# Optimization experiments

Measured on AMD Instinct MI355X. Metric: run time of the kernel, lower is better.

## Reference

```python
import jax, jax.numpy as jnp
import numpy as np

NUM_EXPERTS = 8
INTER = 2816   # moe_intermediate_size
DIM = 1024
T = 16         # flattened tokens
A = 2          # top-k experts per token


def setup_inputs() -> dict:
    key = jax.random.key(0)
    k_x, k_idx, k1, k2, k3 = jax.random.split(key, 5)
    x = jax.random.normal(k_x, (T, DIM), dtype=jnp.float32)
    expert_indices = jax.random.randint(k_idx, (T, A), 0, NUM_EXPERTS, dtype=jnp.int64)
    scale = 0.02
    w1 = jax.random.normal(k1, (NUM_EXPERTS, INTER, DIM), dtype=jnp.float32) * scale
    w2 = jax.random.normal(k2, (NUM_EXPERTS, DIM, INTER), dtype=jnp.float32) * scale
    w3 = jax.random.normal(k3, (NUM_EXPERTS, INTER, DIM), dtype=jnp.float32) * scale
    return {"x": x, "expert_indices": expert_indices, "w1": w1, "w2": w2, "w3": w3}


def reference(x, expert_indices, w1, w2, w3):
    # Gather per-token expert weights (same access pattern as the torch module).
    w1_g = w1[expert_indices]  # [T, A, INTER, DIM]
    w3_g = w3[expert_indices]  # [T, A, INTER, DIM]
    w2_g = w2[expert_indices]  # [T, A, DIM, INTER]
    # SwiGLU: silu(x @ w1^T) * (x @ w3^T), then project back with w2.
    x1 = jax.nn.silu(jnp.einsum('ti,taoi->tao', x, w1_g))  # [T, A, INTER]
    x3 = jnp.einsum('ti,taoi->tao', x, w3_g)               # [T, A, INTER]
    expert_outs = jnp.einsum('tao,taio->tai', x1 * x3, w2_g)  # [T, A, DIM]
    return expert_outs
```

## Files before the change

### kernel.cpp

```cpp
#include <hip/hip_runtime.h>
#include <math.h>

#define TOK   16
#define TOPA  2
#define NPAIR (TOK * TOPA)
#define DIM   1024
#define INTER 2816
#define NEXP  8

__device__ __forceinline__ unsigned pair_mask(const int* __restrict__ eidx, int e) {
    unsigned mask = 0;
    #pragma unroll
    for (int k = 0; k < NPAIR / 4; ++k) {
        const int4 v = ((const int4*)eidx)[k];
        mask |= (unsigned)(v.x == e) << (4 * k + 0);
        mask |= (unsigned)(v.y == e) << (4 * k + 1);
        mask |= (unsigned)(v.z == e) << (4 * k + 2);
        mask |= (unsigned)(v.w == e) << (4 * k + 3);
    }
    return mask;
}

__device__ __forceinline__ float dot4(float4 a, float4 b) {
    return a.x * b.x + a.y * b.y + a.z * b.z + a.w * b.w;
}

__global__ __launch_bounds__(256) void moe_gate_up(
    const float* __restrict__ x,
    const int*   __restrict__ eidx,
    const float* __restrict__ w1,
    const float* __restrict__ w3,
    float*       __restrict__ h)
{
    const int e = blockIdx.y;
    unsigned mask = pair_mask(eidx, e);
    if (!mask) return;

    const int tid  = threadIdx.x;
    const int lane = tid & 63;
    const int wave = tid >> 6;
    const int r0   = blockIdx.x * 8 + wave * 2;

    const float4* w1r = (const float4*)(w1 + ((size_t)e * INTER + r0) * DIM);
    const float4* w3r = (const float4*)(w3 + ((size_t)e * INTER + r0) * DIM);
    const float4* xb  = (const float4*)x;

    while (mask) {
        int p0 = __builtin_ctz(mask); mask &= mask - 1;
        int p1 = p0, p2 = p0, p3 = p0, nv = 1;
        if (mask) { p1 = __builtin_ctz(mask); mask &= mask - 1; nv = 2;
        if (mask) { p2 = __builtin_ctz(mask); mask &= mask - 1; nv = 3;
        if (mask) { p3 = __builtin_ctz(mask); mask &= mask - 1; nv = 4; } } }

        const float4* x0 = xb + (size_t)(p0 >> 1) * (DIM / 4);
        const float4* x1 = xb + (size_t)(p1 >> 1) * (DIM / 4);
        const float4* x2 = xb + (size_t)(p2 >> 1) * (DIM / 4);
        const float4* x3 = xb + (size_t)(p3 >> 1) * (DIM / 4);

        float s1[2][4], s3[2][4];
        #pragma unroll
        for (int r = 0; r < 2; ++r)
            #pragma unroll
            for (int j = 0; j < 4; ++j) { s1[r][j] = 0.f; s3[r][j] = 0.f; }

        #pragma unroll
        for (int k = 0; k < 4; ++k) {
            const float4 a0 = w1r[k * 64 + lane];
            const float4 a1 = w1r[256 + k * 64 + lane];
            const float4 b0 = w3r[k * 64 + lane];
            const float4 b1 = w3r[256 + k * 64 + lane];
            const float4 v0 = x0[k * 64 + lane];
            const float4 v1 = x1[k * 64 + lane];
            const float4 v2 = x2[k * 64 + lane];
            const float4 v3 = x3[k * 64 + lane];
            s1[0][0] += dot4(a0, v0); s1[0][1] += dot4(a0, v1);
            s1[0][2] += dot4(a0, v2); s1[0][3] += dot4(a0, v3);
            s1[1][0] += dot4(a1, v0); s1[1][1] += dot4(a1, v1);
            s1[1][2] += dot4(a1, v2); s1[1][3] += dot4(a1, v3);
            s3[0][0] += dot4(b0, v0); s3[0][1] += dot4(b0, v1);
            s3[0][2] += dot4(b0, v2); s3[0][3] += dot4(b0, v3);
            s3[1][0] += dot4(b1, v0); s3[1][1] += dot4(b1, v1);
            s3[1][2] += dot4(b1, v2); s3[1][3] += dot4(b1, v3);
        }

        #pragma unroll
        for (int off = 1; off < 64; off <<= 1) {
            #pragma unroll
            for (int r = 0; r < 2; ++r)
                #pragma unroll
                for (int j = 0; j < 4; ++j) {
                    s1[r][j] += __shfl_xor(s1[r][j], off);
                    s3[r][j] += __shfl_xor(s3[r][j], off);
                }
        }

        if (lane == 0) {
            const int pp[4] = { p0, p1, p2, p3 };
            #pragma unroll
            for (int j = 0; j < 4; ++j) {
                if (j < nv) {
                    #pragma unroll
                    for (int r = 0; r < 2; ++r) {
                        const float g = s1[r][j] / (1.f + __expf(-s1[r][j]));
                        h[(size_t)pp[j] * INTER + r0 + r] = g * s3[r][j];
                    }
                }
            }
        }
    }
}

__global__ __launch_bounds__(256) void moe_down(
    const float* __restrict__ h,
    const int*   __restrict__ eidx,
    const float* __restrict__ w2,
    float*       __restrict__ out)
{
    const int e = blockIdx.y;
    unsigned mask = pair_mask(eidx, e);
    if (!mask) return;

    const int tid  = threadIdx.x;
    const int lane = tid & 63;
    const int wave = tid >> 6;
    const int r0   = blockIdx.x * 8 + wave * 2;

    const float4* w2r = (const float4*)(w2 + ((size_t)e * DIM + r0) * INTER);
    const float4* hb  = (const float4*)h;

    while (mask) {
        int p0 = __builtin_ctz(mask); mask &= mask - 1;
        int p1 = p0, p2 = p0, p3 = p0, nv = 1;
        if (mask) { p1 = __builtin_ctz(mask); mask &= mask - 1; nv = 2;
        if (mask) { p2 = __builtin_ctz(mask); mask &= mask - 1; nv = 3;
        if (mask) { p3 = __builtin_ctz(mask); mask &= mask - 1; nv = 4; } } }

        const float4* h0 = hb + (size_t)p0 * (INTER / 4);
        const float4* h1 = hb + (size_t)p1 * (INTER / 4);
        const float4* h2 = hb + (size_t)p2 * (INTER / 4);
        const float4* h3 = hb + (size_t)p3 * (INTER / 4);

        float s[2][4];
        #pragma unroll
        for (int r = 0; r < 2; ++r)
            #pragma unroll
            for (int j = 0; j < 4; ++j) s[r][j] = 0.f;

        #pragma unroll
        for (int k = 0; k < 11; ++k) {
            const float4 a0 = w2r[k * 64 + lane];
            const float4 a1 = w2r[704 + k * 64 + lane];
            const float4 v0 = h0[k * 64 + lane];
            const float4 v1 = h1[k * 64 + lane];
            const float4 v2 = h2[k * 64 + lane];
            const float4 v3 = h3[k * 64 + lane];
            s[0][0] += dot4(a0, v0); s[0][1] += dot4(a0, v1);
            s[0][2] += dot4(a0, v2); s[0][3] += dot4(a0, v3);
            s[1][0] += dot4(a1, v0); s[1][1] += dot4(a1, v1);
            s[1][2] += dot4(a1, v2); s[1][3] += dot4(a1, v3);
        }

        #pragma unroll
        for (int off = 1; off < 64; off <<= 1) {
            #pragma unroll
            for (int r = 0; r < 2; ++r)
                #pragma unroll
                for (int j = 0; j < 4; ++j)
                    s[r][j] += __shfl_xor(s[r][j], off);
        }

        if (lane == 0) {
            const int pp[4] = { p0, p1, p2, p3 };
            #pragma unroll
            for (int j = 0; j < 4; ++j) {
                if (j < nv) {
                    #pragma unroll
                    for (int r = 0; r < 2; ++r)
                        out[(size_t)pp[j] * DIM + r0 + r] = s[r][j];
                }
            }
        }
    }
}

extern "C" void kernel_launch(void* const* d_in, const int* in_sizes, int n_in,
                              void* d_out, int out_size, void* d_ws, size_t ws_size,
                              hipStream_t stream) {
    const float* x    = (const float*)d_in[0];
    const int*   eidx = (const int*)  d_in[1];
    const float* w1   = (const float*)d_in[2];
    const float* w2   = (const float*)d_in[3];
    const float* w3   = (const float*)d_in[4];
    float* out = (float*)d_out;
    float* hws = (float*)d_ws;

    dim3 g1(INTER / 8, NEXP);
    moe_gate_up<<<g1, 256, 0, stream>>>(x, eidx, w1, w3, hws);

    dim3 g2(DIM / 8, NEXP);
    moe_down<<<g2, 256, 0, stream>>>(hws, eidx, w2, out);
}
```

Baseline: 65.99 us.

## Stage token rows in LDS, batch 8 pairs, and double-buffer weight loads in gate-up

The gate/up kernel now copies up to 8 token activation rows into shared memory and processes 8 pairs per pass instead of 4. Each block covers 16 rows, with software double-buffered weight loads so the next row's loads overlap the current compute. The reduction becomes a transpose-style butterfly across lanes, so the 16 partial sums finish in fewer shuffles. This halves the number of passes over weights when more than 4 pairs map to an expert, in exchange for block-level syncs, 32KB of LDS per block and a halved grid.

```diff
diff --git a/kernel.cpp b/kernel.cpp
--- a/kernel.cpp
+++ b/kernel.cpp
@@ -3,10 +3,16 @@
 
 #define TOK   16
 #define TOPA  2
-#define NPAIR (TOK * TOPA)
+#define NPAIR 32
 #define DIM   1024
 #define INTER 2816
 #define NEXP  8
+
+#define SLOT(j, m) ((((j) & 1) << 3) | (((j) & 2) << 1) | (((j) & 4) >> 1) | (m))
+
+__device__ __forceinline__ float dot4(float4 a, float4 b) {
+    return a.x * b.x + a.y * b.y + a.z * b.z + a.w * b.w;
+}
 
 __device__ __forceinline__ unsigned pair_mask(const int* __restrict__ eidx, int e) {
     unsigned mask = 0;
@@ -21,92 +27,118 @@
     return mask;
 }
 
-__device__ __forceinline__ float dot4(float4 a, float4 b) {
-    return a.x * b.x + a.y * b.y + a.z * b.z + a.w * b.w;
-}
-
-__global__ __launch_bounds__(256) void moe_gate_up(
-    const float* __restrict__ x,
-    const int*   __restrict__ eidx,
-    const float* __restrict__ w1,
-    const float* __restrict__ w3,
+__global__ __launch_bounds__(256, 4) void moe_gate_up(
+    const float* __restrict__ x,  const int* __restrict__ eidx,
+    const float* __restrict__ w1, const float* __restrict__ w3,
     float*       __restrict__ h)
 {
+    __shared__ float xs[8 * DIM];
+
     const int e = blockIdx.y;
-    unsigned mask = pair_mask(eidx, e);
-    if (!mask) return;
+    unsigned mrem = pair_mask(eidx, e);
+    if (!mrem) return;
 
     const int tid  = threadIdx.x;
     const int lane = tid & 63;
     const int wave = tid >> 6;
-    const int r0   = blockIdx.x * 8 + wave * 2;
-
-    const float4* w1r = (const float4*)(w1 + ((size_t)e * INTER + r0) * DIM);
-    const float4* w3r = (const float4*)(w3 + ((size_t)e * INTER + r0) * DIM);
-    const float4* xb  = (const float4*)x;
-
-    while (mask) {
-        int p0 = __builtin_ctz(mask); mask &= mask - 1;
-        int p1 = p0, p2 = p0, p3 = p0, nv = 1;
-        if (mask) { p1 = __builtin_ctz(mask); mask &= mask - 1; nv = 2;
-        if (mask) { p2 = __builtin_ctz(mask); mask &= mask - 1; nv = 3;
-        if (mask) { p3 = __builtin_ctz(mask); mask &= mask - 1; nv = 4; } } }
-
-        const float4* x0 = xb + (size_t)(p0 >> 1) * (DIM / 4);
-        const float4* x1 = xb + (size_t)(p1 >> 1) * (DIM / 4);
-        const float4* x2 = xb + (size_t)(p2 >> 1) * (DIM / 4);
-        const float4* x3 = xb + (size_t)(p3 >> 1) * (DIM / 4);
-
-        float s1[2][4], s3[2][4];
-        #pragma unroll
-        for (int r = 0; r < 2; ++r)
-            #pragma unroll
-            for (int j = 0; j < 4; ++j) { s1[r][j] = 0.f; s3[r][j] = 0.f; }
-
-        #pragma unroll
-        for (int k = 0; k < 4; ++k) {
-            const float4 a0 = w1r[k * 64 + lane];
-            const float4 a1 = w1r[256 + k * 64 + lane];
-            const float4 b0 = w3r[k * 64 + lane];
-            const float4 b1 = w3r[256 + k * 64 + lane];
-            const float4 v0 = x0[k * 64 + lane];
-            const float4 v1 = x1[k * 64 + lane];
-            const float4 v2 = x2[k * 64 + lane];
-            const float4 v3 = x3[k * 64 + lane];
-            s1[0][0] += dot4(a0, v0); s1[0][1] += dot4(a0, v1);
-            s1[0][2] += dot4(a0, v2); s1[0][3] += dot4(a0, v3);
-            s1[1][0] += dot4(a1, v0); s1[1][1] += dot4(a1, v1);
-            s1[1][2] += dot4(a1, v2); s1[1][3] += dot4(a1, v3);
-            s3[0][0] += dot4(b0, v0); s3[0][1] += dot4(b0, v1);
-            s3[0][2] += dot4(b0, v2); s3[0][3] += dot4(b0, v3);
-            s3[1][0] += dot4(b1, v0); s3[1][1] += dot4(b1, v1);
-            s3[1][2] += dot4(b1, v2); s3[1][3] += dot4(b1, v3);
-        }
-
-        #pragma unroll
-        for (int off = 1; off < 64; off <<= 1) {
-            #pragma unroll
-            for (int r = 0; r < 2; ++r)
-                #pragma unroll
-                for (int j = 0; j < 4; ++j) {
-                    s1[r][j] += __shfl_xor(s1[r][j], off);
-                    s3[r][j] += __shfl_xor(s3[r][j], off);
-                }
-        }
-
-        if (lane == 0) {
-            const int pp[4] = { p0, p1, p2, p3 };
-            #pragma unroll
-            for (int j = 0; j < 4; ++j) {
-                if (j < nv) {
-                    #pragma unroll
-                    for (int r = 0; r < 2; ++r) {
-                        const float g = s1[r][j] / (1.f + __expf(-s1[r][j]));
-                        h[(size_t)pp[j] * INTER + r0 + r] = g * s3[r][j];
-                    }
-                }
-            }
-        }
+    const int r0   = blockIdx.x * 16;
+
+    while (mrem) {
+        int pj[8];
+        const int pfirst = __builtin_ctz(mrem);
+        int npg = 0;
+        #pragma unroll
+        for (int j = 0; j < 8; ++j) {
+            if (mrem) { pj[j] = __builtin_ctz(mrem); mrem &= mrem - 1; ++npg; }
+            else      { pj[j] = pfirst; }
+        }
+
+        const int srow = tid >> 5;
+        int sp = pj[0];
+        #pragma unroll
+        for (int j = 1; j < 8; ++j) if (srow == j) sp = pj[j];
+        __syncthreads();
+        {
+            const int c0 = tid & 31;
+            const float4* src = (const float4*)(x + (size_t)(sp >> 1) * DIM);
+            float4* dst = (float4*)(xs + srow * DIM);
+            #pragma unroll
+            for (int jj = 0; jj < 8; ++jj)
+                dst[c0 + 32 * jj] = src[c0 + 32 * jj];
+        }
+        __syncthreads();
+
+        auto ldw = [&](float4 (&buf)[8], int m) {
+            const int r = r0 + 4 * m + wave;
+            const float4* a = (const float4*)(w1 + ((size_t)e * INTER + r) * DIM);
+            const float4* b = (const float4*)(w3 + ((size_t)e * INTER + r) * DIM);
+            #pragma unroll
+            for (int k = 0; k < 4; ++k) {
+                buf[k]     = a[k * 64 + lane];
+                buf[4 + k] = b[k * 64 + lane];
+            }
+        };
+        auto comp = [&](const float4 (&buf)[8], int m) {
+            float acc[16];
+            #pragma unroll
+            for (int s = 0; s < 16; ++s) acc[s] = 0.f;
+            #pragma unroll
+            for (int k = 0; k < 4; ++k) {
+                #pragma unroll
+                for (int j = 0; j < 8; ++j) {
+                    const float4 xv =
+                        *(const float4*)(xs + j * DIM + (k * 64 + lane) * 4);
+                    acc[SLOT(j, 0)] += dot4(buf[k],     xv);
+                    acc[SLOT(j, 1)] += dot4(buf[4 + k], xv);
+                }
+            }
+            {
+                const bool b0 = lane & 1;
+                #pragma unroll
+                for (int i = 0; i < 8; ++i) {
+                    const float keep = b0 ? acc[i + 8] : acc[i];
+                    const float send = b0 ? acc[i] : acc[i + 8];
+                    acc[i] = keep + __shfl_xor(send, 1);
+                }
+                const bool b1 = lane & 2;
+                #pragma unroll
+                for (int i = 0; i < 4; ++i) {
+                    const float keep = b1 ? acc[i + 4] : acc[i];
+                    const float send = b1 ? acc[i] : acc[i + 4];
+                    acc[i] = keep + __shfl_xor(send, 2);
+                }
+                const bool b2 = lane & 4;
+                #pragma unroll
+                for (int i = 0; i < 2; ++i) {
+                    const float keep = b2 ? acc[i + 2] : acc[i];
+                    const float send = b2 ? acc[i] : acc[i + 2];
+                    acc[i] = keep + __shfl_xor(send, 4);
+                }
+                const bool b3 = lane & 8;
+                {
+                    const float keep = b3 ? acc[1] : acc[0];
+                    const float send = b3 ? acc[0] : acc[1];
+                    acc[0] = keep + __shfl_xor(send, 8);
+                }
+                acc[0] += __shfl_xor(acc[0], 16);
+                acc[0] += __shfl_xor(acc[0], 32);
+            }
+            const float part = __shfl_xor(acc[0], 8);
+            if (lane < npg) {
+                int pp = pj[0];
+                #pragma unroll
+                for (int j = 1; j < 8; ++j) if (lane == j) pp = pj[j];
+                const float g = acc[0] / (1.f + __expf(-acc[0]));
+                h[(size_t)pp * INTER + r0 + 4 * m + wave] = g * part;
+            }
+        };
+
+        float4 A[8], B[8];
+        ldw(A, 0);
+        ldw(B, 1); comp(A, 0);
+        ldw(A, 2); comp(B, 1);
+        ldw(B, 3); comp(A, 2);
+        comp(B, 3);
     }
 }
 
@@ -194,7 +226,7 @@
     float* out = (float*)d_out;
     float* hws = (float*)d_ws;
 
-    dim3 g1(INTER / 8, NEXP);
+    dim3 g1(INTER / 16, NEXP);
     moe_gate_up<<<g1, 256, 0, stream>>>(x, eidx, w1, w3, hws);
 
     dim3 g2(DIM / 8, NEXP);
```

Measured after the change: 113.3 us. 71.7% more time.
